# Kernel tuning notes

Hardware: AMD Instinct MI355X
Metric: run time of the kernel (lower is better)

Reference implementation:

```python
import jax, jax.numpy as jnp
import numpy as np

N = 30000        # nodes
E = 480000       # edges (before self-loops)
F_IN = 1280      # input_features
HID = 64         # hidden_dim
HEADS = 4
C = 2 * HID      # per-head GAT out channels (hidden_dim*2)
NEG_SLOPE = 0.2  # GATConv default negative_slope
EPS = 1e-5       # BatchNorm1d eps


def setup_inputs() -> dict:
    key = jax.random.key(0)
    ks = jax.random.split(key, 8)
    x = jax.random.normal(ks[0], (N, F_IN), jnp.float32)
    edge_index = jax.random.randint(ks[1], (2, E), 0, N)
    edge_weight = jax.random.uniform(ks[2], (E,), jnp.float32)
    W_gat = jax.random.normal(ks[3], (F_IN, HEADS * C), jnp.float32) / np.sqrt(F_IN)
    att_src = jax.random.normal(ks[4], (HEADS, C), jnp.float32) * 0.1
    att_dst = jax.random.normal(ks[5], (HEADS, C), jnp.float32) * 0.1
    b_gat = jnp.zeros((HEADS * C,), jnp.float32)
    bn_gamma = jnp.ones((HEADS * C,), jnp.float32)
    bn_beta = jnp.zeros((HEADS * C,), jnp.float32)
    W_gcn = jax.random.normal(ks[6], (HEADS * C, HID), jnp.float32) / np.sqrt(HEADS * C)
    b_gcn = jnp.zeros((HID,), jnp.float32)
    return dict(x=x, edge_index=edge_index, edge_weight=edge_weight, W_gat=W_gat,
                att_src=att_src, att_dst=att_dst, b_gat=b_gat, bn_gamma=bn_gamma,
                bn_beta=bn_beta, W_gcn=W_gcn, b_gcn=b_gcn)


def _segment_softmax(logits, seg, num):
    m = jax.ops.segment_max(logits, seg, num_segments=num)
    e = jnp.exp(logits - m[seg])
    s = jax.ops.segment_sum(e, seg, num_segments=num)
    return e / (s[seg] + 1e-16)


def reference(x, edge_index, edge_weight, W_gat, att_src, att_dst, b_gat,
              bn_gamma, bn_beta, W_gcn, b_gcn):
    n = x.shape[0]
    loops = jnp.arange(n)
    src = jnp.concatenate([edge_index[0], loops])  # self-loops added by both convs
    dst = jnp.concatenate([edge_index[1], loops])

    # ---- GATConv(F_IN -> HEADS*C, heads=4, concat) ----
    # (edge_weight plays no role: GATConv has edge_dim=None so edge_attr is unused)
    h = (x @ W_gat).reshape(n, HEADS, C)                  # [N,H,C]
    a_src = jnp.einsum('nhc,hc->nh', h, att_src)          # [N,H]
    a_dst = jnp.einsum('nhc,hc->nh', h, att_dst)
    logits = jax.nn.leaky_relu(a_src[src] + a_dst[dst], NEG_SLOPE)  # [E+N,H]
    alpha = _segment_softmax(logits, dst, n)              # softmax over incoming edges
    msg = h[src] * alpha[:, :, None]                      # [E+N,H,C]
    out1 = jax.ops.segment_sum(msg, dst, num_segments=n).reshape(n, HEADS * C) + b_gat

    # ---- BatchNorm1d (training-mode batch stats) + ReLU ----
    mean = out1.mean(axis=0)
    var = out1.var(axis=0)
    xr = jax.nn.relu((out1 - mean) * jax.lax.rsqrt(var + EPS) * bn_gamma + bn_beta)

    # ---- GCNConv(HEADS*C -> HID) with edge_weight, self-loops weight 1 ----
    w = jnp.concatenate([edge_weight, jnp.ones((n,), edge_weight.dtype)])
    deg = jax.ops.segment_sum(w, dst, num_segments=n)
    dinv = jnp.where(deg > 0, jax.lax.rsqrt(deg), 0.0)
    norm = dinv[src] * w * dinv[dst]                      # D^-1/2 A D^-1/2
    h2 = xr @ W_gcn                                       # [N,HID]
    out = jax.ops.segment_sum(h2[src] * norm[:, None], dst, num_segments=n) + b_gcn
    return out
```

## Files before the change

### kernel.cpp

```cpp
#include <hip/hip_runtime.h>
#include <hip/hip_bf16.h>
#include <math.h>

#define N_NODES 30000
#define N_EDGES 480000
#define EE_TOT  510000
#define F_INK   1280
#define HC      512
#define C_PH    128
#define NHID    64

typedef __attribute__((ext_vector_type(8))) short bf16x8;
typedef __attribute__((ext_vector_type(4))) float f32x4;

__device__ inline float wred_max(float v){
  #pragma unroll
  for (int o = 32; o; o >>= 1) v = fmaxf(v, __shfl_xor(v, o));
  return v;
}
__device__ inline float wred_sum(float v){
  #pragma unroll
  for (int o = 32; o; o >>= 1) v += __shfl_xor(v, o);
  return v;
}

__device__ __forceinline__ unsigned short f2bf(float f){
  unsigned u = __float_as_uint(f);
  unsigned r = (u + 0x7FFFu + ((u >> 16) & 1u)) >> 16;
  return (unsigned short)r;
}
__device__ __forceinline__ float b2f(unsigned short s){
  return __uint_as_float((unsigned)s << 16);
}

__device__ __forceinline__ void gld16(const void* g, void* l){
  __builtin_amdgcn_global_load_lds((const __attribute__((address_space(1))) unsigned int*)g,
                                   (__attribute__((address_space(3))) unsigned int*)l, 16, 0, 0);
}

__global__ __launch_bounds__(256) void cvtx(const float* __restrict__ x,
                                            unsigned short* __restrict__ xb){
  size_t i = ((size_t)blockIdx.x * 256 + threadIdx.x) * 4;
  float4 v = *(const float4*)&x[i];
  ushort4 o;
  o.x = f2bf(v.x); o.y = f2bf(v.y); o.z = f2bf(v.z); o.w = f2bf(v.w);
  *(ushort4*)&xb[i] = o;
}

__global__ __launch_bounds__(256) void cvtw(const float* __restrict__ W,
                                            unsigned short* __restrict__ Wb){
  __shared__ float tile[32][33];
  int tx = threadIdx.x & 31, ty = threadIdx.x >> 5;
  int n0 = blockIdx.x * 32, k0 = blockIdx.y * 32;
  #pragma unroll
  for (int i = 0; i < 4; i++){
    int r = ty + i * 8;
    tile[r][tx] = W[(size_t)(k0 + r) * HC + n0 + tx];
  }
  __syncthreads();
  #pragma unroll
  for (int i = 0; i < 4; i++){
    int r = ty + i * 8;
    Wb[(size_t)(n0 + r) * F_INK + k0 + tx] = f2bf(tile[tx][r]);
  }
}

__global__ __launch_bounds__(256) void cvtw2(const float* __restrict__ W,
                                             unsigned short* __restrict__ Wb){
  __shared__ float tile[32][33];
  int tx = threadIdx.x & 31, ty = threadIdx.x >> 5;
  int n0 = blockIdx.x * 32, k0 = blockIdx.y * 32;
  #pragma unroll
  for (int i = 0; i < 4; i++){
    int r = ty + i * 8;
    tile[r][tx] = W[(size_t)(k0 + r) * NHID + n0 + tx];
  }
  __syncthreads();
  #pragma unroll
  for (int i = 0; i < 4; i++){
    int r = ty + i * 8;
    Wb[(size_t)(n0 + r) * HC + k0 + tx] = f2bf(tile[tx][r]);
  }
}

#define BM1 64
#define BN1 256
#define BK 32
#define KTILES (F_INK / BK)
__global__ __launch_bounds__(256) void gemm1_mfma(const unsigned short* __restrict__ A,
                                                  const unsigned short* __restrict__ B,
                                                  unsigned short* __restrict__ C){
  __shared__ __align__(16) unsigned short Ab[2][BM1 * BK];
  __shared__ __align__(16) unsigned short Bb[2][BN1 * BK];
  const int t = threadIdx.x, lane = t & 63, wid = t >> 6;
  const int bm = blockIdx.y * BM1, bn = blockIdx.x * BN1;
  const int r15 = lane & 15;
  const int kq  = (lane >> 4) * 16;
  const int kqs = kq ^ (((r15 >> 1) & 3) << 4);
  const int srow  = (lane >> 2);
  const int skb   = ((lane & 3) * 16) ^ (((lane >> 3) & 3) << 4);

  f32x4 acc[4][4] = {};

  auto stage = [&](int buf, int kt){
    const int k0 = kt * BK;
    {
      int row = wid * 16 + srow;
      int ar = bm + row; if (ar >= N_NODES) ar = N_NODES - 1;
      gld16(&A[(size_t)ar * F_INK + k0 + (skb >> 1)], &Ab[buf][wid * 512]);
    }
    #pragma unroll
    for (int c = 0; c < 4; c++){
      int ch = wid * 4 + c;
      gld16(&B[(size_t)(bn + ch * 16 + srow) * F_INK + k0 + (skb >> 1)], &Bb[buf][ch * 512]);
    }
  };

  stage(0, 0);
  __syncthreads();

  for (int kt = 0; kt < KTILES; kt++){
    const int cur = kt & 1;
    if (kt + 1 < KTILES) stage(cur ^ 1, kt + 1);
    bf16x8 a[4], b[4];
    #pragma unroll
    for (int f = 0; f < 4; f++){
      int rowA = f * 16 + r15;
      a[f] = *(const bf16x8*)((const char*)&Ab[cur][0] + rowA * 64 + kqs);
      int rowB = wid * 64 + f * 16 + r15;
      b[f] = *(const bf16x8*)((const char*)&Bb[cur][0] + rowB * 64 + kqs);
    }
    #pragma unroll
    for (int fm = 0; fm < 4; fm++)
      #pragma unroll
      for (int fn = 0; fn < 4; fn++)
        acc[fm][fn] = __builtin_amdgcn_mfma_f32_16x16x32_bf16(a[fm], b[fn], acc[fm][fn], 0, 0, 0);
    __syncthreads();
  }

  const int ccol0 = bn + wid * 64 + r15;
  #pragma unroll
  for (int fm = 0; fm < 4; fm++){
    #pragma unroll
    for (int j = 0; j < 4; j++){
      int row = bm + fm * 16 + (lane >> 4) * 4 + j;
      if (row < N_NODES){
        #pragma unroll
        for (int fn = 0; fn < 4; fn++)
          C[(size_t)row * HC + ccol0 + fn * 16] = f2bf(acc[fm][fn][j]);
      }
    }
  }
}

__global__ __launch_bounds__(256) void attdot(const unsigned short* __restrict__ hb,
    const float* __restrict__ att_s, const float* __restrict__ att_d,
    float* __restrict__ a_src, float* __restrict__ a_dst){
  int n = blockIdx.x;
  int w = threadIdx.x >> 6;
  int lane = threadIdx.x & 63;
  const unsigned short* hr = hb + (size_t)n * HC + w * C_PH;
  ushort2 hv = *(const ushort2*)(hr + 2 * lane);
  float h0 = b2f(hv.x), h1 = b2f(hv.y);
  const float* as = att_s + w * C_PH;
  const float* ad = att_d + w * C_PH;
  float s1 = h0 * as[2*lane] + h1 * as[2*lane + 1];
  float s2 = h0 * ad[2*lane] + h1 * ad[2*lane + 1];
  s1 = wred_sum(s1); s2 = wred_sum(s2);
  if (lane == 0){ a_src[n*4 + w] = s1; a_dst[n*4 + w] = s2; }
}

__global__ void count_k(const int* __restrict__ ei, int* __restrict__ counts){
  int e = blockIdx.x * 256 + threadIdx.x;
  if (e >= EE_TOT) return;
  int d = (e < N_EDGES) ? ei[N_EDGES + e] : (e - N_EDGES);
  atomicAdd(&counts[d], 1);
}

__global__ __launch_bounds__(1024) void scan_k(const int* __restrict__ counts,
                                               int* __restrict__ offsets){
  __shared__ int sh[1024];
  int t = threadIdx.x;
  int base = t * 30;
  int tot = 0;
  for (int i = 0; i < 30; i++){
    int idx = base + i;
    tot += (idx < N_NODES) ? counts[idx] : 0;
  }
  sh[t] = tot; __syncthreads();
  for (int o = 1; o < 1024; o <<= 1){
    int v = (t >= o) ? sh[t - o] : 0;
    __syncthreads();
    sh[t] += v;
    __syncthreads();
  }
  int run = sh[t] - tot;
  for (int i = 0; i < 30; i++){
    int idx = base + i;
    if (idx < N_NODES){ offsets[idx] = run; run += counts[idx]; }
  }
  if (t == 1023) offsets[N_NODES] = sh[1023];
}

__global__ void fill_k(const int* __restrict__ ei, const float* __restrict__ ew,
                       int* __restrict__ cursor, const int* __restrict__ offsets,
                       int* __restrict__ src_s, float* __restrict__ w_s){
  int e = blockIdx.x * 256 + threadIdx.x;
  if (e >= EE_TOT) return;
  int s, d; float w;
  if (e < N_EDGES){ s = ei[e]; d = ei[N_EDGES + e]; w = ew[e]; }
  else            { s = d = e - N_EDGES; w = 1.0f; }
  int pos = offsets[d] + atomicAdd(&cursor[d], 1);
  src_s[pos] = s; w_s[pos] = w;
}

__global__ __launch_bounds__(64) void attnprep(const int* __restrict__ offsets,
    const int* __restrict__ src_s, const float* __restrict__ w_s,
    const float* __restrict__ a_src, const float* __restrict__ a_dst,
    float* __restrict__ alpha, float* __restrict__ dinv){
  int n = blockIdx.x, lane = threadIdx.x;
  int off = offsets[n], end = offsets[n + 1];
  float4 ad = *(const float4*)&a_dst[n * 4];
  float m0 = -1e30f, m1 = -1e30f, m2 = -1e30f, m3 = -1e30f;
  for (int i = off + lane; i < end; i += 64){
    int s = src_s[i];
    float4 as = *(const float4*)&a_src[s * 4];
    float l0 = as.x + ad.x; l0 = (l0 > 0.f) ? l0 : 0.2f * l0;
    float l1 = as.y + ad.y; l1 = (l1 > 0.f) ? l1 : 0.2f * l1;
    float l2 = as.z + ad.z; l2 = (l2 > 0.f) ? l2 : 0.2f * l2;
    float l3 = as.w + ad.w; l3 = (l3 > 0.f) ? l3 : 0.2f * l3;
    m0 = fmaxf(m0, l0); m1 = fmaxf(m1, l1); m2 = fmaxf(m2, l2); m3 = fmaxf(m3, l3);
  }
  m0 = wred_max(m0); m1 = wred_max(m1); m2 = wred_max(m2); m3 = wred_max(m3);
  float s0 = 0, s1 = 0, s2 = 0, s3 = 0, wsum = 0;
  for (int i = off + lane; i < end; i += 64){
    int s = src_s[i];
    float4 as = *(const float4*)&a_src[s * 4];
    float l0 = as.x + ad.x; l0 = (l0 > 0.f) ? l0 : 0.2f * l0;
    float l1 = as.y + ad.y; l1 = (l1 > 0.f) ? l1 : 0.2f * l1;
    float l2 = as.z + ad.z; l2 = (l2 > 0.f) ? l2 : 0.2f * l2;
    float l3 = as.w + ad.w; l3 = (l3 > 0.f) ? l3 : 0.2f * l3;
    float e0 = expf(l0 - m0), e1 = expf(l1 - m1), e2 = expf(l2 - m2), e3 = expf(l3 - m3);
    float4 av; av.x = e0; av.y = e1; av.z = e2; av.w = e3;
    *(float4*)&alpha[(size_t)i * 4] = av;
    s0 += e0; s1 += e1; s2 += e2; s3 += e3;
    wsum += w_s[i];
  }
  s0 = wred_sum(s0); s1 = wred_sum(s1); s2 = wred_sum(s2); s3 = wred_sum(s3);
  wsum = wred_sum(wsum);
  if (lane == 0) dinv[n] = (wsum > 0.f) ? rsqrtf(wsum) : 0.f;
  float r0 = 1.f / (s0 + 1e-16f), r1 = 1.f / (s1 + 1e-16f);
  float r2 = 1.f / (s2 + 1e-16f), r3 = 1.f / (s3 + 1e-16f);
  for (int i = off + lane; i < end; i += 64){
    float4 av = *(float4*)&alpha[(size_t)i * 4];
    av.x *= r0; av.y *= r1; av.z *= r2; av.w *= r3;
    *(float4*)&alpha[(size_t)i * 4] = av;
  }
}

__global__ __launch_bounds__(256) void gatagg(const int* __restrict__ offsets,
    const int* __restrict__ src_s, const float* __restrict__ alpha,
    const unsigned short* __restrict__ hb, const float* __restrict__ b_gat,
    unsigned short* __restrict__ out1b){
  __shared__ int   s_l[64];
  __shared__ float a_s[64][4];
  int n = blockIdx.x, t = threadIdx.x, wid = t >> 6;
  int off = offsets[n], deg = offsets[n + 1] - off;
  float acc0 = 0, acc1 = 0;
  for (int done = 0; done < deg; done += 64){
    int ce = deg - done; if (ce > 64) ce = 64;
    __syncthreads();
    if (t < 64 && t < ce){
      int idx = off + done + t;
      s_l[t] = src_s[idx];
      float4 av = *(const float4*)&alpha[(size_t)idx * 4];
      a_s[t][0] = av.x; a_s[t][1] = av.y; a_s[t][2] = av.z; a_s[t][3] = av.w;
    }
    __syncthreads();
    for (int i = 0; i < ce; i++){
      const ushort2* hp = (const ushort2*)(hb + (size_t)s_l[i] * HC);
      ushort2 hv = hp[t];
      float a = a_s[i][wid];
      acc0 += b2f(hv.x) * a;
      acc1 += b2f(hv.y) * a;
    }
  }
  ushort2 o;
  o.x = f2bf(acc0 + b_gat[2*t]);
  o.y = f2bf(acc1 + b_gat[2*t + 1]);
  *(ushort2*)&out1b[(size_t)n * HC + 2*t] = o;
}

__global__ __launch_bounds__(256) void bnstats(const unsigned short* __restrict__ out1b,
                                               float* __restrict__ bnacc){
  int t = threadIdx.x;
  float s1 = 0, q1 = 0, s2 = 0, q2 = 0;
  for (int n = blockIdx.x; n < N_NODES; n += gridDim.x){
    ushort2 v = *(const ushort2*)&out1b[(size_t)n * HC + 2*t];
    float v1 = b2f(v.x), v2 = b2f(v.y);
    s1 += v1; q1 += v1 * v1; s2 += v2; q2 += v2 * v2;
  }
  atomicAdd(&bnacc[2*t], s1);      atomicAdd(&bnacc[512 + 2*t], q1);
  atomicAdd(&bnacc[2*t + 1], s2);  atomicAdd(&bnacc[512 + 2*t + 1], q2);
}

__global__ void bnfinal(const float* __restrict__ bnacc, const float* __restrict__ gam,
                        const float* __restrict__ bet, float* __restrict__ bnp){
  int c = blockIdx.x * 256 + threadIdx.x;
  if (c >= 512) return;
  float mean = bnacc[c] * (1.0f / N_NODES);
  float var  = bnacc[512 + c] * (1.0f / N_NODES) - mean * mean;
  float sc = gam[c] * rsqrtf(var + 1e-5f);
  bnp[c] = sc;
  bnp[512 + c] = bet[c] - mean * sc;
}

__global__ __launch_bounds__(256) void bnprep(const unsigned short* __restrict__ out1b,
    const float* __restrict__ bnp, unsigned short* __restrict__ xrb){
  size_t i = ((size_t)blockIdx.x * 256 + threadIdx.x) * 4;
  int c = (int)(i & (HC - 1));
  ushort4 v4 = *(const ushort4*)&out1b[i];
  float4 sc = *(const float4*)&bnp[c];
  float4 sh = *(const float4*)&bnp[512 + c];
  float r; ushort4 o;
  r = b2f(v4.x) * sc.x + sh.x; o.x = f2bf(r > 0.f ? r : 0.f);
  r = b2f(v4.y) * sc.y + sh.y; o.y = f2bf(r > 0.f ? r : 0.f);
  r = b2f(v4.z) * sc.z + sh.z; o.z = f2bf(r > 0.f ? r : 0.f);
  r = b2f(v4.w) * sc.w + sh.w; o.w = f2bf(r > 0.f ? r : 0.f);
  *(ushort4*)&xrb[i] = o;
}

#define BM2 128
#define BK2 32
__global__ __launch_bounds__(256) void gemm2_mfma(const unsigned short* __restrict__ A,
                                                  const unsigned short* __restrict__ B,
                                                  float* __restrict__ C){
  __shared__ __align__(16) unsigned short Ab[2][BM2 * BK2];
  __shared__ __align__(16) unsigned short Bb[2][NHID * BK2];
  const int t = threadIdx.x, lane = t & 63, wid = t >> 6;
  const int bm = blockIdx.x * BM2;
  const int r15 = lane & 15;
  const int kq  = (lane >> 4) * 16;
  const int kqs = kq ^ (((r15 >> 1) & 3) << 4);
  const int srow = lane >> 2;
  const int skb  = ((lane & 3) * 16) ^ (((lane >> 3) & 3) << 4);

  f32x4 acc[2][4] = {};

  auto stage = [&](int buf, int kt){
    const int k0 = kt * BK2;
    #pragma unroll
    for (int c = 0; c < 2; c++){
      int chunk = wid * 2 + c;
      int row = chunk * 16 + srow;
      int ar = bm + row; if (ar >= N_NODES) ar = N_NODES - 1;
      gld16(&A[(size_t)ar * HC + k0 + (skb >> 1)], &Ab[buf][chunk * 512]);
    }
    int rowB = wid * 16 + srow;
    gld16(&B[(size_t)rowB * HC + k0 + (skb >> 1)], &Bb[buf][wid * 512]);
  };

  stage(0, 0);
  __syncthreads();

  #pragma unroll 2
  for (int kt = 0; kt < HC / BK2; kt++){
    const int cur = kt & 1;
    if (kt + 1 < HC / BK2) stage(cur ^ 1, kt + 1);
    bf16x8 a[2], b[4];
    #pragma unroll
    for (int f = 0; f < 2; f++){
      int rowA = wid * 32 + f * 16 + r15;
      a[f] = *(const bf16x8*)((const char*)&Ab[cur][0] + rowA * 64 + kqs);
    }
    #pragma unroll
    for (int f = 0; f < 4; f++){
      int rowB = f * 16 + r15;
      b[f] = *(const bf16x8*)((const char*)&Bb[cur][0] + rowB * 64 + kqs);
    }
    #pragma unroll
    for (int fm = 0; fm < 2; fm++)
      #pragma unroll
      for (int fn = 0; fn < 4; fn++)
        acc[fm][fn] = __builtin_amdgcn_mfma_f32_16x16x32_bf16(a[fm], b[fn], acc[fm][fn], 0, 0, 0);
    __syncthreads();
  }

  #pragma unroll
  for (int fm = 0; fm < 2; fm++){
    #pragma unroll
    for (int j = 0; j < 4; j++){
      int row = bm + wid * 32 + fm * 16 + (lane >> 4) * 4 + j;
      if (row < N_NODES){
        #pragma unroll
        for (int fn = 0; fn < 4; fn++)
          C[(size_t)row * NHID + fn * 16 + r15] = acc[fm][fn][j];
      }
    }
  }
}

__global__ __launch_bounds__(64) void gcnagg(const int* __restrict__ offsets,
    const int* __restrict__ src_s, const float* __restrict__ w_s,
    const float* __restrict__ dinv, const float* __restrict__ h2,
    const float* __restrict__ b_gcn, float* __restrict__ out){
  int n = blockIdx.x, j = threadIdx.x;
  int off = offsets[n], end = offsets[n + 1];
  float dv = dinv[n];
  float acc = 0.f;
  for (int i = off; i < end; i++){
    int s = src_s[i];
    float nrm = dinv[s] * w_s[i] * dv;
    acc += h2[(size_t)s * NHID + j] * nrm;
  }
  out[(size_t)n * NHID + j] = acc + b_gcn[j];
}

extern "C" void kernel_launch(void* const* d_in, const int* in_sizes, int n_in,
                              void* d_out, int out_size, void* d_ws, size_t ws_size,
                              hipStream_t stream){
  const float* x    = (const float*)d_in[0];
  const int*   ei   = (const int*)d_in[1];
  const float* ew   = (const float*)d_in[2];
  const float* Wgat = (const float*)d_in[3];
  const float* atts = (const float*)d_in[4];
  const float* attd = (const float*)d_in[5];
  const float* bgat = (const float*)d_in[6];
  const float* gam  = (const float*)d_in[7];
  const float* bet  = (const float*)d_in[8];
  const float* Wgcn = (const float*)d_in[9];
  const float* bgcn = (const float*)d_in[10];
  float* out = (float*)d_out;

  char* ws = (char*)d_ws;
  size_t cur = 0;
  auto nb = [&](size_t bytes){ cur = (cur + 255) & ~(size_t)255; size_t r = cur; cur += bytes; return r; };
  int*   counts  = (int*)  (ws + nb((size_t)N_NODES * 4));
  int*   cursor  = (int*)  (ws + nb((size_t)N_NODES * 4));
  float* bnacc   = (float*)(ws + nb(1024 * 4));
  size_t zbytes  = cur;
  unsigned short* hb = (unsigned short*)(ws + nb((size_t)N_NODES * HC * 2));
  float* a_src   = (float*)(ws + nb((size_t)N_NODES * 4 * 4));
  float* a_dst   = (float*)(ws + nb((size_t)N_NODES * 4 * 4));
  int*   offsets = (int*)  (ws + nb((size_t)(N_NODES + 1) * 4));
  int*   src_s   = (int*)  (ws + nb((size_t)EE_TOT * 4));
  float* w_s     = (float*)(ws + nb((size_t)EE_TOT * 4));
  size_t reg0    = nb((size_t)EE_TOT * 16);
  size_t reg1    = nb((size_t)N_NODES * HC * 4);
  size_t reg2    = nb((size_t)N_NODES * NHID * 4);
  unsigned short* xb = (unsigned short*)(ws + reg0);
  float* alpha   = (float*)(ws + reg0);
  unsigned short* out1b = (unsigned short*)(ws + reg1);
  float* h2      = (float*)(ws + reg2);
  unsigned short* Wb  = (unsigned short*)(ws + nb((size_t)HC * F_INK * 2));
  unsigned short* Wtb = (unsigned short*)(ws + nb((size_t)NHID * HC * 2));
  unsigned short* xrb = (unsigned short*)(ws + nb((size_t)N_NODES * HC * 2));
  float* bnp     = (float*)(ws + nb(1024 * 4));
  float* dinvp   = (float*)(ws + nb((size_t)N_NODES * 4));
  (void)ws_size; (void)in_sizes; (void)n_in; (void)out_size;

  hipMemsetAsync(d_ws, 0, zbytes, stream);
  count_k <<<(EE_TOT + 255) / 256, 256, 0, stream>>>(ei, counts);
  scan_k  <<<1, 1024, 0, stream>>>(counts, offsets);
  fill_k  <<<(EE_TOT + 255) / 256, 256, 0, stream>>>(ei, ew, cursor, offsets, src_s, w_s);
  cvtx    <<<(N_NODES * F_INK / 4 + 255) / 256, 256, 0, stream>>>(x, xb);
  cvtw    <<<dim3(HC / 32, F_INK / 32), 256, 0, stream>>>(Wgat, Wb);
  cvtw2   <<<dim3(NHID / 32, HC / 32), 256, 0, stream>>>(Wgcn, Wtb);
  gemm1_mfma<<<dim3(HC / BN1, (N_NODES + BM1 - 1) / BM1), 256, 0, stream>>>(xb, Wb, hb);
  attdot  <<<N_NODES, 256, 0, stream>>>(hb, atts, attd, a_src, a_dst);
  attnprep<<<N_NODES, 64, 0, stream>>>(offsets, src_s, w_s, a_src, a_dst, alpha, dinvp);
  gatagg  <<<N_NODES, 256, 0, stream>>>(offsets, src_s, alpha, hb, bgat, out1b);
  bnstats <<<256, 256, 0, stream>>>(out1b, bnacc);
  bnfinal <<<2, 256, 0, stream>>>(bnacc, gam, bet, bnp);
  bnprep  <<<N_NODES * HC / 4 / 256, 256, 0, stream>>>(out1b, bnp, xrb);
  gemm2_mfma<<<(N_NODES + BM2 - 1) / BM2, 256, 0, stream>>>(xrb, Wtb, h2);
  gcnagg  <<<N_NODES, 64, 0, stream>>>(offsets, src_s, w_s, dinvp, h2, bgcn, out);
}
```

Before: 624.3 us.

## Fuse fp32-to-bf16 conversion into GEMM1 and BN+ReLU prologue into GEMM2

Drops the standalone x conversion kernel: GEMM1 now loads fp32 x tiles into registers, converts them to bf16 and writes them to swizzled LDS, overlapping the global load with the MFMA loop. Likewise the BatchNorm apply + ReLU pass is removed and folded into GEMM2's A-tile load path, so the normalized activations are never written to or read back from global memory. This removes roughly two full-size intermediate round trips, but GEMM1 now reads fp32 (twice the bytes) through register staging instead of direct global-to-LDS loads, which adds VGPR pressure and conversion ALU work inside the main loop.

```diff
diff --git a/kernel.cpp b/kernel.cpp
--- a/kernel.cpp
+++ b/kernel.cpp
@@ -38,15 +38,6 @@
                                    (__attribute__((address_space(3))) unsigned int*)l, 16, 0, 0);
 }
 
-__global__ __launch_bounds__(256) void cvtx(const float* __restrict__ x,
-                                            unsigned short* __restrict__ xb){
-  size_t i = ((size_t)blockIdx.x * 256 + threadIdx.x) * 4;
-  float4 v = *(const float4*)&x[i];
-  ushort4 o;
-  o.x = f2bf(v.x); o.y = f2bf(v.y); o.z = f2bf(v.z); o.w = f2bf(v.w);
-  *(ushort4*)&xb[i] = o;
-}
-
 __global__ __launch_bounds__(256) void cvtw(const float* __restrict__ W,
                                             unsigned short* __restrict__ Wb){
   __shared__ float tile[32][33];
@@ -87,7 +78,7 @@
 #define BN1 256
 #define BK 32
 #define KTILES (F_INK / BK)
-__global__ __launch_bounds__(256) void gemm1_mfma(const unsigned short* __restrict__ A,
+__global__ __launch_bounds__(256) void gemm1_mfma(const float* __restrict__ X,
                                                   const unsigned short* __restrict__ B,
                                                   unsigned short* __restrict__ C){
   __shared__ __align__(16) unsigned short Ab[2][BM1 * BK];
@@ -95,20 +86,32 @@
   const int t = threadIdx.x, lane = t & 63, wid = t >> 6;
   const int bm = blockIdx.y * BM1, bn = blockIdx.x * BN1;
   const int r15 = lane & 15;
-  const int kq  = (lane >> 4) * 16;
-  const int kqs = kq ^ (((r15 >> 1) & 3) << 4);
-  const int srow  = (lane >> 2);
-  const int skb   = ((lane & 3) * 16) ^ (((lane >> 3) & 3) << 4);
+  const int kqs = ((lane >> 4) * 16) ^ (((r15 >> 1) & 3) << 4);
+  const int srow = lane >> 2;
+  const int skb  = ((lane & 3) * 16) ^ (((lane >> 3) & 3) << 4);
+  const int arow  = t >> 2;
+  const int aslot = t & 3;
+  const int awby  = arow * 64 + ((aslot ^ ((arow >> 1) & 3)) << 4);
+  int ag = bm + arow; if (ag >= N_NODES) ag = N_NODES - 1;
+  const float* aptr = X + (size_t)ag * F_INK + aslot * 8;
 
   f32x4 acc[4][4] = {};
-
-  auto stage = [&](int buf, int kt){
+  float4 av0, av1;
+
+  auto loadA = [&](int kt){
+    av0 = *(const float4*)(aptr + kt * BK);
+    av1 = *(const float4*)(aptr + kt * BK + 4);
+  };
+  auto writeA = [&](int buf){
+    bf16x8 p;
+    p[0] = (short)f2bf(av0.x); p[1] = (short)f2bf(av0.y);
+    p[2] = (short)f2bf(av0.z); p[3] = (short)f2bf(av0.w);
+    p[4] = (short)f2bf(av1.x); p[5] = (short)f2bf(av1.y);
+    p[6] = (short)f2bf(av1.z); p[7] = (short)f2bf(av1.w);
+    *(bf16x8*)((char*)&Ab[buf][0] + awby) = p;
+  };
+  auto stageB = [&](int buf, int kt){
     const int k0 = kt * BK;
-    {
-      int row = wid * 16 + srow;
-      int ar = bm + row; if (ar >= N_NODES) ar = N_NODES - 1;
-      gld16(&A[(size_t)ar * F_INK + k0 + (skb >> 1)], &Ab[buf][wid * 512]);
-    }
     #pragma unroll
     for (int c = 0; c < 4; c++){
       int ch = wid * 4 + c;
@@ -116,12 +119,12 @@
     }
   };
 
-  stage(0, 0);
+  loadA(0); stageB(0, 0); writeA(0);
   __syncthreads();
 
   for (int kt = 0; kt < KTILES; kt++){
     const int cur = kt & 1;
-    if (kt + 1 < KTILES) stage(cur ^ 1, kt + 1);
+    if (kt + 1 < KTILES){ loadA(kt + 1); stageB(cur ^ 1, kt + 1); }
     bf16x8 a[4], b[4];
     #pragma unroll
     for (int f = 0; f < 4; f++){
@@ -135,6 +138,7 @@
       #pragma unroll
       for (int fn = 0; fn < 4; fn++)
         acc[fm][fn] = __builtin_amdgcn_mfma_f32_16x16x32_bf16(a[fm], b[fn], acc[fm][fn], 0, 0, 0);
+    if (kt + 1 < KTILES) writeA(cur ^ 1);
     __syncthreads();
   }
 
@@ -315,58 +319,70 @@
   bnp[512 + c] = bet[c] - mean * sc;
 }
 
-__global__ __launch_bounds__(256) void bnprep(const unsigned short* __restrict__ out1b,
-    const float* __restrict__ bnp, unsigned short* __restrict__ xrb){
-  size_t i = ((size_t)blockIdx.x * 256 + threadIdx.x) * 4;
-  int c = (int)(i & (HC - 1));
-  ushort4 v4 = *(const ushort4*)&out1b[i];
-  float4 sc = *(const float4*)&bnp[c];
-  float4 sh = *(const float4*)&bnp[512 + c];
-  float r; ushort4 o;
-  r = b2f(v4.x) * sc.x + sh.x; o.x = f2bf(r > 0.f ? r : 0.f);
-  r = b2f(v4.y) * sc.y + sh.y; o.y = f2bf(r > 0.f ? r : 0.f);
-  r = b2f(v4.z) * sc.z + sh.z; o.z = f2bf(r > 0.f ? r : 0.f);
-  r = b2f(v4.w) * sc.w + sh.w; o.w = f2bf(r > 0.f ? r : 0.f);
-  *(ushort4*)&xrb[i] = o;
-}
-
 #define BM2 128
 #define BK2 32
 __global__ __launch_bounds__(256) void gemm2_mfma(const unsigned short* __restrict__ A,
                                                   const unsigned short* __restrict__ B,
+                                                  const float* __restrict__ bnp,
                                                   float* __restrict__ C){
   __shared__ __align__(16) unsigned short Ab[2][BM2 * BK2];
   __shared__ __align__(16) unsigned short Bb[2][NHID * BK2];
   const int t = threadIdx.x, lane = t & 63, wid = t >> 6;
   const int bm = blockIdx.x * BM2;
   const int r15 = lane & 15;
-  const int kq  = (lane >> 4) * 16;
-  const int kqs = kq ^ (((r15 >> 1) & 3) << 4);
+  const int kqs = ((lane >> 4) * 16) ^ (((r15 >> 1) & 3) << 4);
   const int srow = lane >> 2;
   const int skb  = ((lane & 3) * 16) ^ (((lane >> 3) & 3) << 4);
+  const int arow  = t >> 2;
+  const int aslot = t & 3;
+  const int aw0 = arow * 64 + ((aslot ^ ((arow >> 1) & 3)) << 4);
+  const int aw1 = (arow + 64) * 64 + ((aslot ^ (((arow + 64) >> 1) & 3)) << 4);
+  int ag0 = bm + arow;      if (ag0 >= N_NODES) ag0 = N_NODES - 1;
+  int ag1 = bm + arow + 64; if (ag1 >= N_NODES) ag1 = N_NODES - 1;
+  const unsigned short* ap0 = A + (size_t)ag0 * HC + aslot * 8;
+  const unsigned short* ap1 = A + (size_t)ag1 * HC + aslot * 8;
 
   f32x4 acc[2][4] = {};
-
-  auto stage = [&](int buf, int kt){
+  bf16x8 r0, r1; float4 sc0, sc1, sh0, sh1;
+
+  auto loadA = [&](int kt){
     const int k0 = kt * BK2;
-    #pragma unroll
-    for (int c = 0; c < 2; c++){
-      int chunk = wid * 2 + c;
-      int row = chunk * 16 + srow;
-      int ar = bm + row; if (ar >= N_NODES) ar = N_NODES - 1;
-      gld16(&A[(size_t)ar * HC + k0 + (skb >> 1)], &Ab[buf][chunk * 512]);
-    }
+    r0 = *(const bf16x8*)(ap0 + k0);
+    r1 = *(const bf16x8*)(ap1 + k0);
+    int c = k0 + aslot * 8;
+    sc0 = *(const float4*)&bnp[c];       sc1 = *(const float4*)&bnp[c + 4];
+    sh0 = *(const float4*)&bnp[512 + c]; sh1 = *(const float4*)&bnp[512 + c + 4];
+  };
+  auto writeA = [&](int buf){
+    bf16x8 p0, p1;
+    const float* s4a = (const float*)&sc0; const float* s4b = (const float*)&sc1;
+    const float* h4a = (const float*)&sh0; const float* h4b = (const float*)&sh1;
+    #pragma unroll
+    for (int i = 0; i < 4; i++){
+      float v0 = b2f((unsigned short)r0[i])     * s4a[i] + h4a[i];
+      float v1 = b2f((unsigned short)r0[i + 4]) * s4b[i] + h4b[i];
+      p0[i]     = (short)f2bf(v0 > 0.f ? v0 : 0.f);
+      p0[i + 4] = (short)f2bf(v1 > 0.f ? v1 : 0.f);
+      float u0 = b2f((unsigned short)r1[i])     * s4a[i] + h4a[i];
+      float u1 = b2f((unsigned short)r1[i + 4]) * s4b[i] + h4b[i];
+      p1[i]     = (short)f2bf(u0 > 0.f ? u0 : 0.f);
+      p1[i + 4] = (short)f2bf(u1 > 0.f ? u1 : 0.f);
+    }
+    *(bf16x8*)((char*)&Ab[buf][0] + aw0) = p0;
+    *(bf16x8*)((char*)&Ab[buf][0] + aw1) = p1;
+  };
+  auto stageB = [&](int buf, int kt){
+    const int k0 = kt * BK2;
     int rowB = wid * 16 + srow;
     gld16(&B[(size_t)rowB * HC + k0 + (skb >> 1)], &Bb[buf][wid * 512]);
   };
 
-  stage(0, 0);
+  loadA(0); stageB(0, 0); writeA(0);
   __syncthreads();
 
-  #pragma unroll 2
   for (int kt = 0; kt < HC / BK2; kt++){
     const int cur = kt & 1;
-    if (kt + 1 < HC / BK2) stage(cur ^ 1, kt + 1);
+    if (kt + 1 < HC / BK2){ loadA(kt + 1); stageB(cur ^ 1, kt + 1); }
     bf16x8 a[2], b[4];
     #pragma unroll
     for (int f = 0; f < 2; f++){
@@ -383,6 +399,7 @@
       #pragma unroll
       for (int fn = 0; fn < 4; fn++)
         acc[fm][fn] = __builtin_amdgcn_mfma_f32_16x16x32_bf16(a[fm], b[fn], acc[fm][fn], 0, 0, 0);
+    if (kt + 1 < HC / BK2) writeA(cur ^ 1);
     __syncthreads();
   }
 
@@ -439,22 +456,17 @@
   int*   cursor  = (int*)  (ws + nb((size_t)N_NODES * 4));
   float* bnacc   = (float*)(ws + nb(1024 * 4));
   size_t zbytes  = cur;
-  unsigned short* hb = (unsigned short*)(ws + nb((size_t)N_NODES * HC * 2));
+  unsigned short* hb    = (unsigned short*)(ws + nb((size_t)N_NODES * HC * 2));
   float* a_src   = (float*)(ws + nb((size_t)N_NODES * 4 * 4));
   float* a_dst   = (float*)(ws + nb((size_t)N_NODES * 4 * 4));
   int*   offsets = (int*)  (ws + nb((size_t)(N_NODES + 1) * 4));
   int*   src_s   = (int*)  (ws + nb((size_t)EE_TOT * 4));
   float* w_s     = (float*)(ws + nb((size_t)EE_TOT * 4));
-  size_t reg0    = nb((size_t)EE_TOT * 16);
-  size_t reg1    = nb((size_t)N_NODES * HC * 4);
-  size_t reg2    = nb((size_t)N_NODES * NHID * 4);
-  unsigned short* xb = (unsigned short*)(ws + reg0);
-  float* alpha   = (float*)(ws + reg0);
-  unsigned short* out1b = (unsigned short*)(ws + reg1);
-  float* h2      = (float*)(ws + reg2);
+  float* alpha   = (float*)(ws + nb((size_t)EE_TOT * 16));
+  unsigned short* out1b = (unsigned short*)(ws + nb((size_t)N_NODES * HC * 2));
+  float* h2      = (float*)(ws + nb((size_t)N_NODES * NHID * 4));
   unsigned short* Wb  = (unsigned short*)(ws + nb((size_t)HC * F_INK * 2));
   unsigned short* Wtb = (unsigned short*)(ws + nb((size_t)NHID * HC * 2));
-  unsigned short* xrb = (unsigned short*)(ws + nb((size_t)N_NODES * HC * 2));
   float* bnp     = (float*)(ws + nb(1024 * 4));
   float* dinvp   = (float*)(ws + nb((size_t)N_NODES * 4));
   (void)ws_size; (void)in_sizes; (void)n_in; (void)out_size;
@@ -463,16 +475,14 @@
   count_k <<<(EE_TOT + 255) / 256, 256, 0, stream>>>(ei, counts);
   scan_k  <<<1, 1024, 0, stream>>>(counts, offsets);
   fill_k  <<<(EE_TOT + 255) / 256, 256, 0, stream>>>(ei, ew, cursor, offsets, src_s, w_s);
-  cvtx    <<<(N_NODES * F_INK / 4 + 255) / 256, 256, 0, stream>>>(x, xb);
   cvtw    <<<dim3(HC / 32, F_INK / 32), 256, 0, stream>>>(Wgat, Wb);
   cvtw2   <<<dim3(NHID / 32, HC / 32), 256, 0, stream>>>(Wgcn, Wtb);
-  gemm1_mfma<<<dim3(HC / BN1, (N_NODES + BM1 - 1) / BM1), 256, 0, stream>>>(xb, Wb, hb);
+  gemm1_mfma<<<dim3(HC / BN1, (N_NODES + BM1 - 1) / BM1), 256, 0, stream>>>(x, Wb, hb);
   attdot  <<<N_NODES, 256, 0, stream>>>(hb, atts, attd, a_src, a_dst);
   attnprep<<<N_NODES, 64, 0, stream>>>(offsets, src_s, w_s, a_src, a_dst, alpha, dinvp);
   gatagg  <<<N_NODES, 256, 0, stream>>>(offsets, src_s, alpha, hb, bgat, out1b);
   bnstats <<<256, 256, 0, stream>>>(out1b, bnacc);
   bnfinal <<<2, 256, 0, stream>>>(bnacc, gam, bet, bnp);
-  bnprep  <<<N_NODES * HC / 4 / 256, 256, 0, stream>>>(out1b, bnp, xrb);
-  gemm2_mfma<<<(N_NODES + BM2 - 1) / BM2, 256, 0, stream>>>(xrb, Wtb, h2);
+  gemm2_mfma<<<(N_NODES + BM2 - 1) / BM2, 256, 0, stream>>>(out1b, Wtb, bnp, h2);
   gcnagg  <<<N_NODES, 64, 0, stream>>>(offsets, src_s, w_s, dinvp, h2, bgcn, out);
 }
```

Result: no change. 629.5 us (+0.8%).
